# Performance work log

Hardware: AMD Instinct MI355X
Metric: run time of the kernel (lower is better)

## Reference

```python
import jax, jax.numpy as jnp
import numpy as np

IMAGE_SIZE = 1024      # config.model.image_size
DOWNSIZING = 64        # PromptGetter grid cell size (in upsampled pixels)
THRESHOLD = 0.65       # default_threshold_target
NUM_BG = 1             # num_bg_points
EPS = 1e-12


def setup_inputs() -> dict:
    key = jax.random.key(0)
    k1, k2 = jax.random.split(key)
    image_embeddings = jax.random.normal(k1, (1, 256, 64, 64), dtype=jnp.float32)
    reference_feats = jax.random.normal(k2, (32, 1, 256), dtype=jnp.float32)
    return {"image_embeddings": image_embeddings, "reference_feats": reference_feats}


def _point_selection(sim_up):
    """sim_up: [S, S] similarity map at original resolution.
    Returns (points_scores [n_cells, 3] as (x, y, score) sorted by score desc,
             bg_coords [NUM_BG, 2] as (x, y)).
    Faithful static-shape version of PromptGetter._point_selection: the torch
    code picks, within every DOWNSIZING x DOWNSIZING grid cell, the highest-sim
    pixel above threshold; cells with no pixel above threshold yield -1 rows."""
    n = IMAGE_SIZE // DOWNSIZING  # 16 -> 256 grid cells
    # background point: global minimum of the similarity map
    flat = sim_up.reshape(-1)
    _, bg_idx = jax.lax.top_k(-flat, NUM_BG)
    bg_row = bg_idx // IMAGE_SIZE
    bg_col = bg_idx % IMAGE_SIZE
    bg_coords = jnp.stack([bg_col, bg_row], axis=-1).astype(jnp.float32)  # (x, y)

    # foreground: per-grid-cell argmax
    cells = sim_up.reshape(n, DOWNSIZING, n, DOWNSIZING)
    cells = cells.transpose(0, 2, 1, 3).reshape(n * n, DOWNSIZING * DOWNSIZING)
    local_idx = jnp.argmax(cells, axis=-1)                                   # [n*n]
    score = jnp.take_along_axis(cells, local_idx[:, None], axis=-1)[:, 0]    # [n*n]
    cell_ids = jnp.arange(n * n)
    cy, cx = cell_ids // n, cell_ids % n
    ly, lx = local_idx // DOWNSIZING, local_idx % DOWNSIZING
    y = (cy * DOWNSIZING + ly).astype(jnp.float32)
    x = (cx * DOWNSIZING + lx).astype(jnp.float32)
    pts = jnp.stack([x, y, score], axis=-1)                                   # [n*n, 3]
    valid = score > THRESHOLD
    pts = jnp.where(valid[:, None], pts, jnp.float32(-1.0))
    order = jnp.argsort(-pts[:, 2])  # sort by score, descending; -1 rows sink
    return pts[order], bg_coords


def reference(image_embeddings, reference_feats):
    # image_embeddings: [1, C, h, w]; reference_feats: [L, 1, C]
    feat = image_embeddings[0]                                   # [C, h, w]
    C, h, w = feat.shape
    feat = feat / (jnp.linalg.norm(feat, axis=0, keepdims=True) + EPS)
    feat = feat.reshape(C, h * w)                                # [C, h*w]
    ref = reference_feats[:, 0, :]                               # [L, C]
    ref = ref / (jnp.linalg.norm(ref, axis=-1, keepdims=True) + EPS)
    sim = (ref @ feat).reshape(-1, h, w)                         # [L, h, w] cosine sim
    # postprocess_masks with original_size == image_size: one bilinear upsample
    sim_up = jax.image.resize(sim, (sim.shape[0], IMAGE_SIZE, IMAGE_SIZE), method="bilinear")
    total_points_scores, total_bg_coords = jax.vmap(_point_selection)(sim_up)
    return total_points_scores, total_bg_coords
```

## Files before the change

### kernel.cpp

```cpp
#include <hip/hip_runtime.h>
#include <math.h>

#define THRESH 0.65f


__global__ __launch_bounds__(256) void k_sim(const float* __restrict__ feat,
                                             const float* __restrict__ ref,
                                             float* __restrict__ sim) {
    __shared__ float rnS[2][256];
    __shared__ float red[256];
    int t = threadIdx.x;
    int m0 = blockIdx.y * 2;

    float v0 = ref[m0 * 256 + t];
    float v1 = ref[(m0 + 1) * 256 + t];
    red[t] = v0 * v0;
    __syncthreads();
    for (int s = 128; s > 0; s >>= 1) { if (t < s) red[t] += red[t + s]; __syncthreads(); }
    float den0 = sqrtf(red[0]) + 1e-12f;
    __syncthreads();
    red[t] = v1 * v1;
    __syncthreads();
    for (int s = 128; s > 0; s >>= 1) { if (t < s) red[t] += red[t + s]; __syncthreads(); }
    float den1 = sqrtf(red[0]) + 1e-12f;
    rnS[0][t] = v0 / den0;
    rnS[1][t] = v1 / den1;
    __syncthreads();

    int px = blockIdx.x * 128 + (t >> 1);
    int mi = t & 1;
    const float* fp = feat + px;
    const float* rn = rnS[mi];
    float dot = 0.f, nsq = 0.f;
    for (int g = 0; g < 16; ++g) {
        float p = 0.f, nq = 0.f;
#pragma unroll
        for (int cc = 0; cc < 16; ++cc) {
            int c = g * 16 + cc;
            float fv = fp[c * 4096];
            p += fv * rn[c];
            nq += fv * fv;
        }
        dot += p; nsq += nq;
    }
    sim[(m0 + mi) * 4096 + px] = dot / (sqrtf(nsq) + 1e-12f);
}

__global__ __launch_bounds__(256) void k_scan(const float* __restrict__ sim,
                                              float* __restrict__ cellscore,
                                              int* __restrict__ cellidx,
                                              float* __restrict__ bgval,
                                              int* __restrict__ bgidx) {
    __shared__ float S[6 * 19];
    __shared__ float wmin[4];
    __shared__ int wmini[4];

    int t = threadIdx.x;
    int bx = blockIdx.x;
    int cy = bx >> 2, qx = bx & 3;
    int m = blockIdx.y;
    int ybase = 4 * cy - 1;
    int xgbase = 16 * qx - 1;
    const float* sm = sim + m * 4096;

    if (t < 108) {
        int j = t / 18, col = t - 18 * j;
        int gy = min(max(ybase + j, 0), 63);
        int gx = min(max(xgbase + col, 0), 63);
        S[j * 19 + col] = sm[gy * 64 + gx];
    }
    __syncthreads();

    int cxl = t >> 6, r = t & 63;
    int cx = qx * 4 + cxl;
    int oy = cy * 64 + r;
    float fy = (oy + 0.5f) * 0.0625f - 0.5f;
    float y0f = floorf(fy);
    float wy = fy - y0f;
    bool ylo = fy < 0.0f, yhi = fy > 63.0f;
    int y0 = (int)y0f;
    int py0 = min(max(y0, 0), 63) - ybase;
    int py1 = min(max(y0 + 1, 0), 63) - ybase;
    const float* P0 = S + py0 * 19;
    const float* P1 = S + py1 * 19;
    float w1y = 1.0f - wy;

    const int   L0[5]  = {0, 8, 24, 40, 56};
    const int   L1[5]  = {7, 23, 39, 55, 63};
    const float WXA[5] = {0.53125f, 0.03125f, 0.03125f, 0.03125f, 0.03125f};
    const float WXB[5] = {0.96875f, 0.96875f, 0.96875f, 0.96875f, 0.46875f};
    const float WCA[5] = {0.46875f, 0.96875f, 0.96875f, 0.96875f, 0.96875f};
    const float WCB[5] = {0.03125f, 0.03125f, 0.03125f, 0.03125f, 0.53125f};

    bool xlo = (cx == 0), xhi = (cx == 15);
    float bmax = -1e30f; int bmaxi = 0;
    float bmin = 1e30f;  int bmini = 0;
    int libase = r * 64;
    int rowbase = oy * 1024 + cx * 64;

#pragma unroll
    for (int s5 = 0; s5 < 5; ++s5) {
        int i0 = 4 * cxl + s5;
        float a = P0[i0], b = P0[i0 + 1];
        float c = P1[i0], d = P1[i0 + 1];
        float q0 = ylo ? a : (yhi ? c : w1y * a + wy * c);
        float q1 = ylo ? b : (yhi ? d : w1y * b + wy * d);
        float va, vb;
        if (xlo && s5 == 0)      { va = q1; vb = q1; }
        else if (xhi && s5 == 4) { va = q0; vb = q0; }
        else {
            va = WCA[s5] * q0 + WXA[s5] * q1;
            vb = WCB[s5] * q0 + WXB[s5] * q1;
        }
        float smax, smin; int smaxl, sminl;
        if (va >= vb) { smax = va; smaxl = L0[s5]; } else { smax = vb; smaxl = L1[s5]; }
        if (va <= vb) { smin = va; sminl = L0[s5]; } else { smin = vb; sminl = L1[s5]; }
        if (smax > bmax) { bmax = smax; bmaxi = libase + smaxl; }
        if (smin < bmin) { bmin = smin; bmini = rowbase + sminl; }
    }

    for (int off = 32; off > 0; off >>= 1) {
        float ov = __shfl_down(bmax, off);
        int   oi = __shfl_down(bmaxi, off);
        if (ov > bmax || (ov == bmax && oi < bmaxi)) { bmax = ov; bmaxi = oi; }
        float mv = __shfl_down(bmin, off);
        int   mj = __shfl_down(bmini, off);
        if (mv < bmin || (mv == bmin && mj < bmini)) { bmin = mv; bmini = mj; }
    }
    if (r == 0) {
        int cell = cy * 16 + cx;
        cellscore[m * 256 + cell] = bmax;
        cellidx[m * 256 + cell] = bmaxi;
        wmin[cxl] = bmin;
        wmini[cxl] = bmini;
    }
    __syncthreads();
    if (t == 0) {
        float bv = wmin[0]; int bi = wmini[0];
        for (int w = 1; w < 4; ++w) {
            if (wmin[w] < bv || (wmin[w] == bv && wmini[w] < bi)) {
                bv = wmin[w]; bi = wmini[w];
            }
        }
        bgval[m * 64 + bx] = bv;
        bgidx[m * 64 + bx] = bi;
    }
}

__global__ __launch_bounds__(256) void k_out(const float* __restrict__ cellscore,
                                             const int* __restrict__ cellidx,
                                             const float* __restrict__ bgval,
                                             const int* __restrict__ bgidx,
                                             float* __restrict__ out) {
    __shared__ float sc[256];
    __shared__ float mv[64];
    __shared__ int mi_[64];
    int m = blockIdx.x, t = threadIdx.x;
    float score = cellscore[m * 256 + t];
    int li = cellidx[m * 256 + t];
    int cy = t >> 4, cx = t & 15;
    int ly = li >> 6, lx = li & 63;
    bool valid = score > THRESH;
    float px = valid ? (float)(cx * 64 + lx) : -1.0f;
    float py = valid ? (float)(cy * 64 + ly) : -1.0f;
    float ps = valid ? score : -1.0f;
    sc[t] = ps;
    if (t < 64) { mv[t] = bgval[m * 64 + t]; mi_[t] = bgidx[m * 64 + t]; }
    __syncthreads();
    int rank = 0;
    for (int j = 0; j < 256; ++j) {
        float sj = sc[j];
        rank += (sj > ps || (sj == ps && j < t)) ? 1 : 0;
    }
    float* o = out + m * 768 + rank * 3;
    o[0] = px; o[1] = py; o[2] = ps;
    for (int s = 32; s > 0; s >>= 1) {
        __syncthreads();
        if (t < s) {
            float v2 = mv[t + s]; int i2 = mi_[t + s];
            if (v2 < mv[t] || (v2 == mv[t] && i2 < mi_[t])) { mv[t] = v2; mi_[t] = i2; }
        }
    }
    __syncthreads();
    if (t == 0) {
        int bi = mi_[0];
        out[24576 + m * 2 + 0] = (float)(bi % 1024);
        out[24576 + m * 2 + 1] = (float)(bi / 1024);
    }
}

extern "C" void kernel_launch(void* const* d_in, const int* in_sizes, int n_in,
                              void* d_out, int out_size, void* d_ws, size_t ws_size,
                              hipStream_t stream) {
    const float* feat = (const float*)d_in[0];
    const float* ref  = (const float*)d_in[1];
    if (in_sizes[0] == 32 * 256) {
        feat = (const float*)d_in[1];
        ref  = (const float*)d_in[0];
    }
    float* out = (float*)d_out;
    float* ws = (float*)d_ws;
    float* sim       = ws;
    float* cellscore = ws + 131072;
    int*   cellidx   = (int*)(ws + 139264);
    float* bgval     = ws + 147456;
    int*   bgidx     = (int*)(ws + 149504);

    k_sim<<<dim3(32, 16), 256, 0, stream>>>(feat, ref, sim);
    k_scan<<<dim3(64, 32), 256, 0, stream>>>(sim, cellscore, cellidx, bgval, bgidx);
    k_out<<<32, 256, 0, stream>>>(cellscore, cellidx, bgval, bgidx, out);
}
```

Before: 79.49 us.

## Fuse scan and output kernels, split channel reduction across thread halves in k_sim

k_scan and k_out are merged into one kernel with one block per reference map. The whole 64x64 sim map is staged in padded shared memory, and each thread scans one grid cell over its candidate rows and columns before doing the rank sort and background min in place. This removes a launch and the workspace round trip. In k_sim, each thread now computes both reference dot products for one pixel over half the channels, so each feature load is reused twice, and a shared-memory add combines the halves. The cost is that the fused kernel runs only 32 blocks, with each thread doing more serial work (about 10 rows x 6 loads), which lowers parallelism on a large GPU.

```diff
diff --git a/kernel.cpp b/kernel.cpp
--- a/kernel.cpp
+++ b/kernel.cpp
@@ -7,8 +7,8 @@
 __global__ __launch_bounds__(256) void k_sim(const float* __restrict__ feat,
                                              const float* __restrict__ ref,
                                              float* __restrict__ sim) {
-    __shared__ float rnS[2][256];
-    __shared__ float red[256];
+    __shared__ float rn0[256], rn1[256], red[256];
+    __shared__ float pd0[256], pd1[256], pn[256];
     int t = threadIdx.x;
     int m0 = blockIdx.y * 2;
 
@@ -23,68 +23,57 @@
     __syncthreads();
     for (int s = 128; s > 0; s >>= 1) { if (t < s) red[t] += red[t + s]; __syncthreads(); }
     float den1 = sqrtf(red[0]) + 1e-12f;
-    rnS[0][t] = v0 / den0;
-    rnS[1][t] = v1 / den1;
+    rn0[t] = v0 / den0;
+    rn1[t] = v1 / den1;
     __syncthreads();
 
-    int px = blockIdx.x * 128 + (t >> 1);
-    int mi = t & 1;
-    const float* fp = feat + px;
-    const float* rn = rnS[mi];
-    float dot = 0.f, nsq = 0.f;
-    for (int g = 0; g < 16; ++g) {
-        float p = 0.f, nq = 0.f;
+    int half = t >> 7, pxl = t & 127;
+    int px = blockIdx.x * 128 + pxl;
+    const float* fp = feat + px + half * 128 * 4096;
+    const float* r0 = rn0 + half * 128;
+    const float* r1 = rn1 + half * 128;
+    float d0 = 0.f, d1 = 0.f, nq = 0.f;
+    for (int g = 0; g < 8; ++g) {
 #pragma unroll
         for (int cc = 0; cc < 16; ++cc) {
             int c = g * 16 + cc;
             float fv = fp[c * 4096];
-            p += fv * rn[c];
+            d0 += fv * r0[c];
+            d1 += fv * r1[c];
             nq += fv * fv;
         }
-        dot += p; nsq += nq;
     }
-    sim[(m0 + mi) * 4096 + px] = dot / (sqrtf(nsq) + 1e-12f);
+    pd0[t] = d0; pd1[t] = d1; pn[t] = nq;
+    __syncthreads();
+    float D0 = pd0[pxl] + pd0[pxl + 128];
+    float D1 = pd1[pxl] + pd1[pxl + 128];
+    float NQ = pn[pxl] + pn[pxl + 128];
+    float den = sqrtf(NQ) + 1e-12f;
+    sim[(m0 + half) * 4096 + px] = (half ? D1 : D0) / den;
 }
 
-__global__ __launch_bounds__(256) void k_scan(const float* __restrict__ sim,
-                                              float* __restrict__ cellscore,
-                                              int* __restrict__ cellidx,
-                                              float* __restrict__ bgval,
-                                              int* __restrict__ bgidx) {
-    __shared__ float S[6 * 19];
+__global__ __launch_bounds__(256) void k_scan_out(const float* __restrict__ sim,
+                                                  float* __restrict__ out) {
+    __shared__ float S[64 * 65];
+    __shared__ float sc[256];
     __shared__ float wmin[4];
     __shared__ int wmini[4];
 
-    int t = threadIdx.x;
-    int bx = blockIdx.x;
-    int cy = bx >> 2, qx = bx & 3;
-    int m = blockIdx.y;
-    int ybase = 4 * cy - 1;
-    int xgbase = 16 * qx - 1;
+    int m = blockIdx.x, t = threadIdx.x;
     const float* sm = sim + m * 4096;
-
-    if (t < 108) {
-        int j = t / 18, col = t - 18 * j;
-        int gy = min(max(ybase + j, 0), 63);
-        int gx = min(max(xgbase + col, 0), 63);
-        S[j * 19 + col] = sm[gy * 64 + gx];
+    for (int k = 0; k < 16; ++k) {
+        int f = t + 256 * k;
+        S[(f >> 6) * 65 + (f & 63)] = sm[f];
     }
     __syncthreads();
 
-    int cxl = t >> 6, r = t & 63;
-    int cx = qx * 4 + cxl;
-    int oy = cy * 64 + r;
-    float fy = (oy + 0.5f) * 0.0625f - 0.5f;
-    float y0f = floorf(fy);
-    float wy = fy - y0f;
-    bool ylo = fy < 0.0f, yhi = fy > 63.0f;
-    int y0 = (int)y0f;
-    int py0 = min(max(y0, 0), 63) - ybase;
-    int py1 = min(max(y0 + 1, 0), 63) - ybase;
-    const float* P0 = S + py0 * 19;
-    const float* P1 = S + py1 * 19;
-    float w1y = 1.0f - wy;
-
+    int cy = t >> 4, cx = t & 15;
+    int gxs[6];
+#pragma unroll
+    for (int j = 0; j < 6; ++j) {
+        int g = 4 * cx - 1 + j;
+        gxs[j] = min(max(g, 0), 63);
+    }
     const int   L0[5]  = {0, 8, 24, 40, 56};
     const int   L1[5]  = {7, 23, 39, 55, 63};
     const float WXA[5] = {0.53125f, 0.03125f, 0.03125f, 0.03125f, 0.03125f};
@@ -92,48 +81,66 @@
     const float WCA[5] = {0.46875f, 0.96875f, 0.96875f, 0.96875f, 0.96875f};
     const float WCB[5] = {0.03125f, 0.03125f, 0.03125f, 0.03125f, 0.53125f};
 
-    bool xlo = (cx == 0), xhi = (cx == 15);
-    float bmax = -1e30f; int bmaxi = 0;
-    float bmin = 1e30f;  int bmini = 0;
-    int libase = r * 64;
-    int rowbase = oy * 1024 + cx * 64;
-
+    float bmax = -1e30f, bmin = 1e30f;
+    int bmaxi = 0, bmini = 0;
 #pragma unroll
-    for (int s5 = 0; s5 < 5; ++s5) {
-        int i0 = 4 * cxl + s5;
-        float a = P0[i0], b = P0[i0 + 1];
-        float c = P1[i0], d = P1[i0 + 1];
-        float q0 = ylo ? a : (yhi ? c : w1y * a + wy * c);
-        float q1 = ylo ? b : (yhi ? d : w1y * b + wy * d);
-        float va, vb;
-        if (xlo && s5 == 0)      { va = q1; vb = q1; }
-        else if (xhi && s5 == 4) { va = q0; vb = q0; }
-        else {
-            va = WCA[s5] * q0 + WXA[s5] * q1;
-            vb = WCB[s5] * q0 + WXB[s5] * q1;
+    for (int sy = 0; sy < 5; ++sy) {
+#pragma unroll
+        for (int e = 0; e < 2; ++e) {
+            int r = e ? L1[sy] : L0[sy];
+            int oy = cy * 64 + r;
+            float fy = (oy + 0.5f) * 0.0625f - 0.5f;
+            float y0f = floorf(fy);
+            float wy = fy - y0f, w1y = 1.0f - wy;
+            bool ylo = fy < 0.0f, yhi = fy > 63.0f;
+            int y0 = (int)y0f;
+            const float* P0 = S + min(max(y0, 0), 63) * 65;
+            const float* P1 = S + min(max(y0 + 1, 0), 63) * 65;
+            float q[6];
+#pragma unroll
+            for (int j = 0; j < 6; ++j) {
+                float a = P0[gxs[j]], c = P1[gxs[j]];
+                q[j] = ylo ? a : (yhi ? c : w1y * a + wy * c);
+            }
+#pragma unroll
+            for (int s5 = 0; s5 < 5; ++s5) {
+                float q0 = q[s5], q1 = q[s5 + 1];
+                float va, vb;
+                if (cx == 0 && s5 == 0)       { va = q1; vb = q1; }
+                else if (cx == 15 && s5 == 4) { va = q0; vb = q0; }
+                else {
+                    va = WCA[s5] * q0 + WXA[s5] * q1;
+                    vb = WCB[s5] * q0 + WXB[s5] * q1;
+                }
+                float smax, smin; int smaxl, sminl;
+                if (va >= vb) { smax = va; smaxl = L0[s5]; } else { smax = vb; smaxl = L1[s5]; }
+                if (va <= vb) { smin = va; sminl = L0[s5]; } else { smin = vb; sminl = L1[s5]; }
+                if (smax > bmax) { bmax = smax; bmaxi = r * 64 + smaxl; }
+                if (smin < bmin) { bmin = smin; bmini = oy * 1024 + cx * 64 + sminl; }
+            }
         }
-        float smax, smin; int smaxl, sminl;
-        if (va >= vb) { smax = va; smaxl = L0[s5]; } else { smax = vb; smaxl = L1[s5]; }
-        if (va <= vb) { smin = va; sminl = L0[s5]; } else { smin = vb; sminl = L1[s5]; }
-        if (smax > bmax) { bmax = smax; bmaxi = libase + smaxl; }
-        if (smin < bmin) { bmin = smin; bmini = rowbase + sminl; }
     }
 
+    bool valid = bmax > THRESH;
+    float px = valid ? (float)(cx * 64 + (bmaxi & 63)) : -1.0f;
+    float py = valid ? (float)(cy * 64 + (bmaxi >> 6)) : -1.0f;
+    float ps = valid ? bmax : -1.0f;
+    sc[t] = ps;
+    __syncthreads();
+    int rank = 0;
+    for (int j = 0; j < 256; ++j) {
+        float sj = sc[j];
+        rank += (sj > ps || (sj == ps && j < t)) ? 1 : 0;
+    }
+    float* o = out + m * 768 + rank * 3;
+    o[0] = px; o[1] = py; o[2] = ps;
+
     for (int off = 32; off > 0; off >>= 1) {
-        float ov = __shfl_down(bmax, off);
-        int   oi = __shfl_down(bmaxi, off);
-        if (ov > bmax || (ov == bmax && oi < bmaxi)) { bmax = ov; bmaxi = oi; }
         float mv = __shfl_down(bmin, off);
         int   mj = __shfl_down(bmini, off);
         if (mv < bmin || (mv == bmin && mj < bmini)) { bmin = mv; bmini = mj; }
     }
-    if (r == 0) {
-        int cell = cy * 16 + cx;
-        cellscore[m * 256 + cell] = bmax;
-        cellidx[m * 256 + cell] = bmaxi;
-        wmin[cxl] = bmin;
-        wmini[cxl] = bmini;
-    }
+    if ((t & 63) == 0) { wmin[t >> 6] = bmin; wmini[t >> 6] = bmini; }
     __syncthreads();
     if (t == 0) {
         float bv = wmin[0]; int bi = wmini[0];
@@ -142,48 +149,6 @@
                 bv = wmin[w]; bi = wmini[w];
             }
         }
-        bgval[m * 64 + bx] = bv;
-        bgidx[m * 64 + bx] = bi;
-    }
-}
-
-__global__ __launch_bounds__(256) void k_out(const float* __restrict__ cellscore,
-                                             const int* __restrict__ cellidx,
-                                             const float* __restrict__ bgval,
-                                             const int* __restrict__ bgidx,
-                                             float* __restrict__ out) {
-    __shared__ float sc[256];
-    __shared__ float mv[64];
-    __shared__ int mi_[64];
-    int m = blockIdx.x, t = threadIdx.x;
-    float score = cellscore[m * 256 + t];
-    int li = cellidx[m * 256 + t];
-    int cy = t >> 4, cx = t & 15;
-    int ly = li >> 6, lx = li & 63;
-    bool valid = score > THRESH;
-    float px = valid ? (float)(cx * 64 + lx) : -1.0f;
-    float py = valid ? (float)(cy * 64 + ly) : -1.0f;
-    float ps = valid ? score : -1.0f;
-    sc[t] = ps;
-    if (t < 64) { mv[t] = bgval[m * 64 + t]; mi_[t] = bgidx[m * 64 + t]; }
-    __syncthreads();
-    int rank = 0;
-    for (int j = 0; j < 256; ++j) {
-        float sj = sc[j];
-        rank += (sj > ps || (sj == ps && j < t)) ? 1 : 0;
-    }
-    float* o = out + m * 768 + rank * 3;
-    o[0] = px; o[1] = py; o[2] = ps;
-    for (int s = 32; s > 0; s >>= 1) {
-        __syncthreads();
-        if (t < s) {
-            float v2 = mv[t + s]; int i2 = mi_[t + s];
-            if (v2 < mv[t] || (v2 == mv[t] && i2 < mi_[t])) { mv[t] = v2; mi_[t] = i2; }
-        }
-    }
-    __syncthreads();
-    if (t == 0) {
-        int bi = mi_[0];
         out[24576 + m * 2 + 0] = (float)(bi % 1024);
         out[24576 + m * 2 + 1] = (float)(bi / 1024);
     }
@@ -199,14 +164,8 @@
         ref  = (const float*)d_in[0];
     }
     float* out = (float*)d_out;
-    float* ws = (float*)d_ws;
-    float* sim       = ws;
-    float* cellscore = ws + 131072;
-    int*   cellidx   = (int*)(ws + 139264);
-    float* bgval     = ws + 147456;
-    int*   bgidx     = (int*)(ws + 149504);
+    float* sim = (float*)d_ws;
 
     k_sim<<<dim3(32, 16), 256, 0, stream>>>(feat, ref, sim);
-    k_scan<<<dim3(64, 32), 256, 0, stream>>>(sim, cellscore, cellidx, bgval, bgidx);
-    k_out<<<32, 256, 0, stream>>>(cellscore, cellidx, bgval, bgidx, out);
+    k_scan_out<<<32, 256, 0, stream>>>(sim, out);
 }
```

Result: faster. 74.24 us (-6.6%).
